# Performance work log

Hardware: AMD Instinct MI355X
Metric: run time of the kernel (lower is better)

The kernel has to match this reference:

```python
import jax, jax.numpy as jnp
import numpy as np

NEG = -1e30  # finite stand-in for -inf (safe under grads)


def setup_inputs() -> dict:
    key = jax.random.key(0)
    k0, k1, k2, k3 = jax.random.split(key, 4)
    B, L, NS, NG = 32, 1024, 32768, 64
    spans = jax.random.randint(k0, (B, NS, 2), 0, L)
    span_scores = jax.random.normal(k1, (B, NS), dtype=jnp.float32)
    gold_spans = jax.random.randint(k2, (B, NG, 2), 0, L)
    gold_span_labels = jax.random.randint(k3, (B, NG), 0, 2)
    span_mask = jnp.ones((B, NS), jnp.float32)
    gold_span_mask = jnp.ones((B, NG), jnp.float32)
    token_mask = jnp.ones((B, L), jnp.float32)
    return {
        "spans": spans,
        "span_scores": span_scores,
        "gold_spans": gold_spans,
        "gold_span_labels": gold_span_labels,
        "span_mask": span_mask,
        "gold_span_mask": gold_span_mask,
        "token_mask": token_mask,
    }


def _span_table(spans, span_scores, L):
    # T[b, s, e] = sum of span_scores over list entries with (start, end) == (s, e)
    B = span_scores.shape[0]
    b = jnp.arange(B)[:, None]
    T = jnp.zeros((B, L, L), span_scores.dtype)
    return T.at[b, spans[..., 0], spans[..., 1]].add(span_scores)


def _log_denominator(T, token_mask):
    # semi-Markov CRF forward algorithm.
    # beta[i] = logsumexp over last-segment-start j of alpha[i, j]; the original
    # DP only consumes alpha rows through their row-logsumexp, so:
    # beta[i] = logsumexp({beta[s] + S(s, i-1) : s < i} U {beta[i-1] - S(i-1, i-1)})
    B, L = token_mask.shape

    def step(beta, i):
        row = jax.lax.dynamic_index_in_dim(T, i - 1, axis=2, keepdims=False)  # (B, L): S(s, i-1)
        valid = jnp.arange(L) < i
        cand = jnp.where(valid[None, :], beta[:, :L] + row, NEG)
        lse_plus = jax.nn.logsumexp(cand, axis=1)                             # (B,)
        beta_prev = jax.lax.dynamic_index_in_dim(beta, i - 1, axis=1, keepdims=False)
        diag = jax.lax.dynamic_index_in_dim(row, i - 1, axis=1, keepdims=False)  # S(i-1, i-1)
        new_val = jnp.logaddexp(lse_plus, beta_prev - diag)
        beta = jax.lax.dynamic_update_index_in_dim(beta, new_val, i, axis=1)
        return beta, None

    beta0 = jnp.full((B, L + 1), NEG, T.dtype).at[:, 0].set(0.0)
    beta, _ = jax.lax.scan(step, beta0, jnp.arange(1, L + 1))
    n = token_mask.sum(-1).astype(jnp.int32)  # valid length per batch element
    return jnp.take_along_axis(beta, n[:, None], axis=1)[:, 0]


def _log_numerator(T, gold_spans, gold_span_labels, gold_span_mask):
    B = T.shape[0]
    b = jnp.arange(B)[:, None]
    vals = T[b, gold_spans[..., 0], gold_spans[..., 1]]  # (B, NG)
    signs = 2.0 * gold_span_labels.astype(T.dtype) - 1.0
    return jnp.sum(vals * gold_span_mask * signs, axis=1)


def reference(spans, span_scores, gold_spans, gold_span_labels, span_mask, gold_span_mask, token_mask):
    # span_mask is accepted (as in the original forward signature) but unused
    # by the likelihood math in the source.
    L = token_mask.shape[1]
    T = _span_table(spans, span_scores, L)
    log_den = _log_denominator(T, token_mask)
    log_num = _log_numerator(T, gold_spans, gold_span_labels, gold_span_mask)
    return jnp.sum(log_num - log_den)
```

## Files before the change

### kernel.cpp

```cpp
#include <hip/hip_runtime.h>


#define B_   32
#define L_   1024
#define NS_  32768
#define NG_  64
#define CAP_ 128

#define DPP_ADD(v, ctrl) \
    ((v) + __int_as_float(__builtin_amdgcn_update_dpp( \
        0, __float_as_int(v), (ctrl), 0xf, 0xf, false)))

__device__ __forceinline__ float wave_sum64(float v) {
    v = DPP_ADD(v, 0x111);
    v = DPP_ADD(v, 0x112);
    v = DPP_ADD(v, 0x114);
    v = DPP_ADD(v, 0x118);
    v = DPP_ADD(v, 0x142);
    v = DPP_ADD(v, 0x143);
    return __int_as_float(__builtin_amdgcn_readlane(__float_as_int(v), 63));
}

__global__ void __launch_bounds__(256) sbc_scatter(
        const int2* __restrict__ spans, const float* __restrict__ scores,
        const int2* __restrict__ gold,  const int* __restrict__ labels,
        const float* __restrict__ gmask,
        unsigned int* __restrict__ keys, float* __restrict__ vals,
        float* __restrict__ num) {
    const int j = blockIdx.x;
    const int b = j & 31;
    const int tid = threadIdx.x;
    __shared__ unsigned int hkey[128];
    __shared__ float hval[128];
    __shared__ int slotof[NG_];
    if (tid < 128) { hkey[tid] = 0u; hval[tid] = 0.f; }
    __syncthreads();
    if (tid < NG_) {
        int2 se = gold[b * NG_ + tid];
        unsigned cell = ((unsigned)se.x << 10) | (unsigned)se.y;
        unsigned key = cell + 1u;
        unsigned h = (cell * 2654435761u) >> 25;
        int slot = 0;
        for (int p = 0; p < 128; ++p) {
            unsigned old = atomicCAS(&hkey[h], 0u, key);
            if (old == 0u || old == key) { slot = (int)h; break; }
            h = (h + 1u) & 127u;
        }
        slotof[tid] = slot;
    }
    __syncthreads();
    #pragma unroll
    for (int r = 0; r < 4; ++r) {
        const int gi = (b << 15) + ((j >> 5) << 10) + (r << 8) + tid;
        int2 se = spans[gi];
        float sc = scores[gi];
        {
            unsigned cell = ((unsigned)se.x << 10) | (unsigned)se.y;
            unsigned key = cell + 1u;
            unsigned h = (cell * 2654435761u) >> 25;
            for (int p = 0; p < 128; ++p) {
                unsigned k = hkey[h];
                if (k == 0u) break;
                if (k == key) { atomicAdd(&hval[h], sc); break; }
                h = (h + 1u) & 127u;
            }
        }
        if (se.x <= se.y) {
            size_t col = ((size_t)b << 10) | (unsigned)se.y;
            unsigned int* kcol = keys + col * CAP_;
            float*        vcol = vals + col * CAP_;
            unsigned key = (unsigned)se.x + 1u;
            int h = se.x & (CAP_ - 1);
            for (int p = 0; p < CAP_; ++p) {
                unsigned old = atomicCAS(&kcol[h], 0u, key);
                if (old == 0u || old == key) { atomicAdd(&vcol[h], sc); break; }
                h = (h + 1) & (CAP_ - 1);
            }
        }
    }
    __syncthreads();
    if (tid < NG_) {
        int g = b * NG_ + tid;
        float acc = hval[slotof[tid]] * gmask[g] * (2.f * (float)labels[g] - 1.f);
        #pragma unroll
        for (int o = 32; o; o >>= 1) acc += __shfl_xor(acc, o, 64);
        if (tid == 0) atomicAdd(&num[b], acc);
    }
}

__global__ void __launch_bounds__(256) sbc_prep(const unsigned int* __restrict__ keys,
                                                const float* __restrict__ vals,
                                                uint2* __restrict__ rec) {
    const int j = blockIdx.x;
    const int b = j & 31;
    const int cb = (j >> 5) * 16;
    const int wv = threadIdx.x >> 6;
    const int lane = threadIdx.x & 63;
    __shared__ uint2 st[4][CAP_];
    __shared__ float dnr[4][8];
    for (int cc = 0; cc < 4; ++cc) {
        const int e = cb + wv * 4 + cc;
        const size_t col = ((size_t)b << 10) | (unsigned)e;
        const unsigned int* kcol = keys + col * CAP_;
        const float*        vcol = vals + col * CAP_;
        ((uint4*)st[wv])[lane] = make_uint4(0u, 0u, 0u, 0u);
        if (lane < 8) dnr[wv][lane] = 0.f;
        int cnt = 0;
        #pragma unroll
        for (int r = 0; r < 2; ++r) {
            int slot = lane + r * 64;
            unsigned k = kcol[slot];
            float v = vcol[slot];
            bool occ = (k != 0u);
            int s = (int)k - 1;
            int t = e - s;
            if (occ && t <= 3) atomicAdd(&dnr[wv][t], v);
            bool far = occ && (t >= 4);
            unsigned long long mb = __ballot(far);
            int pos = cnt + (int)__popcll(mb & ((1ull << lane) - 1ull));
            if (far && pos < CAP_ - 2)
                st[wv][2 + pos] = make_uint2((unsigned)s, __float_as_uint(expm1f(v)));
            cnt += (int)__popcll(mb);
        }
        if (lane == 0) {
            float d = dnr[wv][0];
            st[wv][0] = make_uint2(__float_as_uint(__expf(d) + __expf(-d) - 1.f),
                                   __float_as_uint(expm1f(dnr[wv][1])));
            st[wv][1] = make_uint2(__float_as_uint(expm1f(dnr[wv][2])),
                                   __float_as_uint(expm1f(dnr[wv][3])));
        }
        ((uint4*)(rec + col * CAP_))[lane] = ((const uint4*)st[wv])[lane];
    }
}

__global__ void __launch_bounds__(64) sbc_dp(const uint2* __restrict__ rec,
                                             const float* __restrict__ tmask,
                                             float* __restrict__ den) {
    const int b = blockIdx.x;
    const int lane = threadIdx.x;
    __shared__ float xs[L_ + 1];
    const uint4* pb = (const uint4*)rec + (size_t)b * L_ * 64;

    for (int t = lane; t <= L_; t += 64) xs[t] = 0.f;
    if (lane == 0) xs[0] = 1.f;

    float tm = 0.f;
    for (int t = lane; t < L_; t += 64) tm += tmask[b * L_ + t];
    #pragma unroll
    for (int o = 32; o; o >>= 1) tm += __shfl_xor(tm, o, 64);
    int n = (int)(tm + 0.5f);
    n = (n > L_) ? L_ : n;

    uint4 metaS[4];
    #pragma unroll
    for (int c = 0; c < 4; ++c) metaS[c] = pb[c * 64 + lane];
    uint4 pkS[8];
    #pragma unroll
    for (int k = 0; k < 8; ++k) pkS[(4 + k) & 7] = pb[(4 + k) * 64 + lane];

    float gX0[4] = {0,0,0,0}, gX1[4] = {0,0,0,0};
    float gW0[4] = {0,0,0,0}, gW1[4] = {0,0,0,0};
    float Kcur = 0.f;
    float P = 1.f, m = 0.f;
    float xm1 = 1.f, xm2 = 0.f, xm3 = 0.f, xm4 = 0.f;
    const bool gl = (lane >= 1);

    for (int ii = 0; ii < L_; ii += 8) {
        #pragma unroll
        for (int Kc = 0; Kc < 8; ++Kc) {
            const int e = ii + Kc;
            const int cs = (Kc + 1) & 3;
            float p = gW0[cs] * gX0[cs] + gW1[cs] * gX1[cs];
            float Knext = wave_sum64(p);
            uint4 M = metaS[Kc & 3];
            uint4 pk = pkS[(Kc + 4) & 7];
            metaS[Kc & 3] = pk;
            int s0 = (int)(pk.x & 1023u);
            int s1 = (int)(pk.z & 1023u);
            gX0[Kc & 3] = xs[s0];
            gX1[Kc & 3] = xs[s1];
            gW0[Kc & 3] = gl ? __uint_as_float(pk.y) : 0.f;
            gW1[Kc & 3] = gl ? __uint_as_float(pk.w) : 0.f;
            int cl = e + 12; cl = (cl > L_ - 1) ? (L_ - 1) : cl;
            pkS[(Kc + 4) & 7] = pb[cl * 64 + lane];
            float A = (P + Kcur)
                    + (__uint_as_float(M.y) * xm2 + __uint_as_float(M.z) * xm3)
                    + __uint_as_float(M.w) * xm4;
            float x = fmaf(xm1, __uint_as_float(M.x), A);
            if (lane == 0) xs[e + 1] = x;
            P += x;
            unsigned long long bm = __ballot(x > 0x1p64f);
            if (bm & 1ull) {
                const float s_ = 0x1p-64f;
                x *= s_; xm1 *= s_; xm2 *= s_; xm3 *= s_;
                P *= s_; Knext *= s_;
                #pragma unroll
                for (int q = 0; q < 4; ++q) { gX0[q] *= s_; gX1[q] *= s_; }
                m += 44.361419555836498f;
                for (int jj = lane; jj <= e + 1; jj += 64) xs[jj] *= s_;
            }
            xm4 = xm3; xm3 = xm2; xm2 = xm1; xm1 = x;
            Kcur = Knext;
        }
    }
    if (lane == 0) den[b] = m + logf(xs[n]);
}

__global__ void sbc_final(const float* __restrict__ num,
                          const float* __restrict__ den,
                          float* __restrict__ out) {
    int lane = threadIdx.x;
    float v = (lane < B_) ? (num[lane] - den[lane]) : 0.f;
    #pragma unroll
    for (int o = 32; o; o >>= 1) v += __shfl_xor(v, o, 64);
    if (lane == 0) out[0] = v;
}

extern "C" void kernel_launch(void* const* d_in, const int* in_sizes, int n_in,
                              void* d_out, int out_size, void* d_ws, size_t ws_size,
                              hipStream_t stream) {
    const int2*  spans       = (const int2*)d_in[0];
    const float* span_scores = (const float*)d_in[1];
    const int2*  gold        = (const int2*)d_in[2];
    const int*   glabels     = (const int*)d_in[3];
    const float* gmask       = (const float*)d_in[5];
    const float* tmask       = (const float*)d_in[6];
    float* out = (float*)d_out;
    (void)in_sizes; (void)n_in; (void)out_size; (void)ws_size;

    char* ws = (char*)d_ws;
    const size_t keysB = (size_t)B_ * L_ * CAP_ * 4;
    const size_t valsB = keysB;
    unsigned int* keys = (unsigned int*)(ws);
    float*        vals = (float*)(ws + keysB);
    float*        num  = (float*)(ws + keysB + valsB);
    float*        den  = num + B_;
    uint2*        recp = (uint2*)(ws + keysB + valsB + 256);

    hipMemsetAsync(keys, 0, keysB + valsB + B_ * 4, stream);
    sbc_scatter<<<1024, 256, 0, stream>>>(spans, span_scores, gold, glabels,
                                          gmask, keys, vals, num);
    sbc_prep<<<2048, 256, 0, stream>>>(keys, vals, recp);
    sbc_dp<<<B_, 64, 0, stream>>>(recp, tmask, den);
    sbc_final<<<1, 64, 0, stream>>>(num, den, out);
}
```

Before: 328.5 us.

## Pack two batch DPs into one wave using half-wave reductions

The semi-Markov DP kernel now runs two batch elements per 64-lane wave. Each 32-lane half owns one batch and its own LDS prefix array, and each lane gathers four record entries per step instead of two. The full-wave DPP reduction with readlane becomes a half-wave DPP reduction followed by a shuffle broadcast. Rescaling is applied per half. This halves the number of waves, but it lengthens each serial step: twice the LDS gathers per lane, a bpermute instead of readlane, and rescale branches triggered by either batch.

```diff
diff --git a/kernel.cpp b/kernel.cpp
--- a/kernel.cpp
+++ b/kernel.cpp
@@ -11,14 +11,13 @@
     ((v) + __int_as_float(__builtin_amdgcn_update_dpp( \
         0, __float_as_int(v), (ctrl), 0xf, 0xf, false)))
 
-__device__ __forceinline__ float wave_sum64(float v) {
+__device__ __forceinline__ float half_bcast_sum(float v, int lane) {
     v = DPP_ADD(v, 0x111);
     v = DPP_ADD(v, 0x112);
     v = DPP_ADD(v, 0x114);
     v = DPP_ADD(v, 0x118);
     v = DPP_ADD(v, 0x142);
-    v = DPP_ADD(v, 0x143);
-    return __int_as_float(__builtin_amdgcn_readlane(__float_as_int(v), 63));
+    return __shfl(v, (lane & 32) + 31, 64);
 }
 
 __global__ void __launch_bounds__(256) sbc_scatter(
@@ -136,74 +135,87 @@
 __global__ void __launch_bounds__(64) sbc_dp(const uint2* __restrict__ rec,
                                              const float* __restrict__ tmask,
                                              float* __restrict__ den) {
-    const int b = blockIdx.x;
     const int lane = threadIdx.x;
-    __shared__ float xs[L_ + 1];
-    const uint4* pb = (const uint4*)rec + (size_t)b * L_ * 64;
-
-    for (int t = lane; t <= L_; t += 64) xs[t] = 0.f;
-    if (lane == 0) xs[0] = 1.f;
+    const int sl   = lane & 31;
+    const int half = lane >> 5;
+    const int batch = (blockIdx.x & 7) + ((blockIdx.x >> 3) << 4) + (half << 3);
+    __shared__ float xs2[2][L_ + 1];
+    float* xsh = xs2[half];
+    const uint4* pb = (const uint4*)rec + (size_t)batch * L_ * 64;
+
+    for (int t = sl; t <= L_; t += 32) xsh[t] = 0.f;
+    if (sl == 0) xsh[0] = 1.f;
 
     float tm = 0.f;
-    for (int t = lane; t < L_; t += 64) tm += tmask[b * L_ + t];
-    #pragma unroll
-    for (int o = 32; o; o >>= 1) tm += __shfl_xor(tm, o, 64);
+    for (int t = sl; t < L_; t += 32) tm += tmask[batch * L_ + t];
+    tm = half_bcast_sum(tm, lane);
     int n = (int)(tm + 0.5f);
     n = (n > L_) ? L_ : n;
 
     uint4 metaS[4];
     #pragma unroll
-    for (int c = 0; c < 4; ++c) metaS[c] = pb[c * 64 + lane];
-    uint4 pkS[8];
-    #pragma unroll
-    for (int k = 0; k < 8; ++k) pkS[(4 + k) & 7] = pb[(4 + k) * 64 + lane];
-
-    float gX0[4] = {0,0,0,0}, gX1[4] = {0,0,0,0};
-    float gW0[4] = {0,0,0,0}, gW1[4] = {0,0,0,0};
+    for (int c = 0; c < 4; ++c) metaS[c] = pb[c * 64 + sl];
+    uint4 pkS0[8], pkS1[8];
+    #pragma unroll
+    for (int k = 0; k < 8; ++k) {
+        pkS0[(4 + k) & 7] = pb[(4 + k) * 64 + sl];
+        pkS1[(4 + k) & 7] = pb[(4 + k) * 64 + 32 + sl];
+    }
+
+    float gX0[4]={0,0,0,0}, gX1[4]={0,0,0,0}, gX2[4]={0,0,0,0}, gX3[4]={0,0,0,0};
+    float gW0[4]={0,0,0,0}, gW1[4]={0,0,0,0}, gW2[4]={0,0,0,0}, gW3[4]={0,0,0,0};
     float Kcur = 0.f;
     float P = 1.f, m = 0.f;
     float xm1 = 1.f, xm2 = 0.f, xm3 = 0.f, xm4 = 0.f;
-    const bool gl = (lane >= 1);
+    const bool gl = (sl >= 1);
 
     for (int ii = 0; ii < L_; ii += 8) {
         #pragma unroll
         for (int Kc = 0; Kc < 8; ++Kc) {
             const int e = ii + Kc;
             const int cs = (Kc + 1) & 3;
-            float p = gW0[cs] * gX0[cs] + gW1[cs] * gX1[cs];
-            float Knext = wave_sum64(p);
+            float p = gW0[cs]*gX0[cs] + gW1[cs]*gX1[cs]
+                    + gW2[cs]*gX2[cs] + gW3[cs]*gX3[cs];
+            float Knext = half_bcast_sum(p, lane);
             uint4 M = metaS[Kc & 3];
-            uint4 pk = pkS[(Kc + 4) & 7];
-            metaS[Kc & 3] = pk;
-            int s0 = (int)(pk.x & 1023u);
-            int s1 = (int)(pk.z & 1023u);
-            gX0[Kc & 3] = xs[s0];
-            gX1[Kc & 3] = xs[s1];
-            gW0[Kc & 3] = gl ? __uint_as_float(pk.y) : 0.f;
-            gW1[Kc & 3] = gl ? __uint_as_float(pk.w) : 0.f;
+            uint4 pk0 = pkS0[(Kc + 4) & 7];
+            uint4 pk1 = pkS1[(Kc + 4) & 7];
+            metaS[Kc & 3] = pk0;
+            gX0[Kc & 3] = xsh[(int)(pk0.x & 1023u)];
+            gX1[Kc & 3] = xsh[(int)(pk0.z & 1023u)];
+            gX2[Kc & 3] = xsh[(int)(pk1.x & 1023u)];
+            gX3[Kc & 3] = xsh[(int)(pk1.z & 1023u)];
+            gW0[Kc & 3] = gl ? __uint_as_float(pk0.y) : 0.f;
+            gW1[Kc & 3] = gl ? __uint_as_float(pk0.w) : 0.f;
+            gW2[Kc & 3] = __uint_as_float(pk1.y);
+            gW3[Kc & 3] = __uint_as_float(pk1.w);
             int cl = e + 12; cl = (cl > L_ - 1) ? (L_ - 1) : cl;
-            pkS[(Kc + 4) & 7] = pb[cl * 64 + lane];
+            pkS0[(Kc + 4) & 7] = pb[cl * 64 + sl];
+            pkS1[(Kc + 4) & 7] = pb[cl * 64 + 32 + sl];
             float A = (P + Kcur)
                     + (__uint_as_float(M.y) * xm2 + __uint_as_float(M.z) * xm3)
                     + __uint_as_float(M.w) * xm4;
             float x = fmaf(xm1, __uint_as_float(M.x), A);
-            if (lane == 0) xs[e + 1] = x;
+            if (sl == 0) xsh[e + 1] = x;
             P += x;
             unsigned long long bm = __ballot(x > 0x1p64f);
-            if (bm & 1ull) {
-                const float s_ = 0x1p-64f;
+            if (bm & 0x100000001ull) {
+                unsigned nb = (unsigned)(bm >> (lane & 32)) & 1u;
+                float s_ = nb ? 0x1p-64f : 1.f;
                 x *= s_; xm1 *= s_; xm2 *= s_; xm3 *= s_;
                 P *= s_; Knext *= s_;
                 #pragma unroll
-                for (int q = 0; q < 4; ++q) { gX0[q] *= s_; gX1[q] *= s_; }
-                m += 44.361419555836498f;
-                for (int jj = lane; jj <= e + 1; jj += 64) xs[jj] *= s_;
+                for (int q = 0; q < 4; ++q) {
+                    gX0[q]*=s_; gX1[q]*=s_; gX2[q]*=s_; gX3[q]*=s_;
+                }
+                m += nb ? 44.361419555836498f : 0.f;
+                for (int jj = sl; jj <= e + 1; jj += 32) xsh[jj] *= s_;
             }
             xm4 = xm3; xm3 = xm2; xm2 = xm1; xm1 = x;
             Kcur = Knext;
         }
     }
-    if (lane == 0) den[b] = m + logf(xs[n]);
+    if (sl == 0) den[batch] = m + logf(xsh[n]);
 }
 
 __global__ void sbc_final(const float* __restrict__ num,
@@ -241,6 +253,6 @@
     sbc_scatter<<<1024, 256, 0, stream>>>(spans, span_scores, gold, glabels,
                                           gmask, keys, vals, num);
     sbc_prep<<<2048, 256, 0, stream>>>(keys, vals, recp);
-    sbc_dp<<<B_, 64, 0, stream>>>(recp, tmask, den);
+    sbc_dp<<<16, 64, 0, stream>>>(recp, tmask, den);
     sbc_final<<<1, 64, 0, stream>>>(num, den, out);
 }
```

Result: slower. 371.8 us (+13.2%).
